# Optimization experiments

Hardware: AMD Instinct MI355X
Metric: run time of the kernel (lower is better)

The kernel has to match this reference:

```python
import jax, jax.numpy as jnp
import numpy as np

N_NODES = 50000
N_EDGES = 600000
D_IN = 128
D_HID = 128


def _sage_conv(x, src, dst, W_l, b_l, W_r):
    """PyG SAGEConv (mean aggr): out = lin_l(mean_{j in N(i)} x_j) + lin_r(x_i).
    bias lives in lin_l only."""
    n = x.shape[0]
    agg = jax.ops.segment_sum(x[src], dst, num_segments=n)            # [N, D]
    cnt = jax.ops.segment_sum(jnp.ones((src.shape[0],), x.dtype), dst, num_segments=n)
    mean = agg / jnp.maximum(cnt, 1.0)[:, None]
    return mean @ W_l.T + b_l + x @ W_r.T


def setup_inputs() -> dict:
    key = jax.random.key(0)
    ks = jax.random.split(key, 8)
    glorot = lambda k, o, i: jax.random.normal(k, (o, i), jnp.float32) * np.sqrt(2.0 / (o + i))
    return {
        "x": jax.random.normal(ks[0], (N_NODES, D_IN), jnp.float32),
        "edge_index": jax.random.randint(ks[1], (2, N_EDGES), 0, N_NODES, jnp.int64),
        "W1_l": glorot(ks[2], D_HID, D_IN),
        "b1": jnp.zeros((D_HID,), jnp.float32),
        "W1_r": glorot(ks[3], D_HID, D_IN),
        "W2_l": glorot(ks[4], D_HID, D_HID),
        "b2": jnp.zeros((D_HID,), jnp.float32),
        "W2_r": glorot(ks[5], D_HID, D_HID),
    }


def reference(x, edge_index, W1_l, b1, W1_r, W2_l, b2, W2_r):
    src, dst = edge_index[0], edge_index[1]
    h = _sage_conv(x, src, dst, W1_l, b1, W1_r)
    h = jax.nn.leaky_relu(h, negative_slope=0.2)
    return _sage_conv(h, src, dst, W2_l, b2, W2_r)
```

## Files before the change

kernel.cpp:

```cpp
#include <hip/hip_runtime.h>

#define N_NODES 50000
#define N_EDGES 600000
#define D 128
#define CAP 32
#define NTILES (N_NODES / 16)

typedef __attribute__((ext_vector_type(8))) short bf16x8;
typedef __attribute__((ext_vector_type(4))) float floatx4;
typedef __attribute__((ext_vector_type(2))) float f32x2;

__device__ inline unsigned int f2bf(float f) {
    unsigned int u = __float_as_uint(f);
    return (u + 0x7FFFu + ((u >> 16) & 1u)) >> 16;
}
__device__ inline float bf_lo(unsigned int u) { return __uint_as_float(u << 16); }
__device__ inline float bf_hi(unsigned int u) { return __uint_as_float(u & 0xFFFF0000u); }

__global__ void k_prep(const float* __restrict__ x, unsigned short* __restrict__ xbf,
                       const float* __restrict__ wa, const float* __restrict__ wb,
                       const float* __restrict__ wc, const float* __restrict__ wd,
                       unsigned short* __restrict__ wbf,
                       const int* __restrict__ src, const int* __restrict__ dst,
                       int* __restrict__ cnt, unsigned short* __restrict__ buf,
                       int* __restrict__ spillN, unsigned int* __restrict__ spillP) {
    const int b = blockIdx.x;
    const int t = threadIdx.x;
    if (b < 586) {
        int idx = b * 256 + t;
        if (idx * 4 < N_EDGES) {
            int4 dv = ((const int4*)dst)[idx];
            int4 sv = ((const int4*)src)[idx];
            int p0 = atomicAdd(&cnt[dv.x], 1);
            int p1 = atomicAdd(&cnt[dv.y], 1);
            int p2 = atomicAdd(&cnt[dv.z], 1);
            int p3 = atomicAdd(&cnt[dv.w], 1);
            if (p0 < CAP) buf[(size_t)dv.x * CAP + p0] = (unsigned short)sv.x;
            else { int k = atomicAdd(spillN, 1); spillP[k] = ((unsigned)dv.x << 16) | (unsigned)sv.x; }
            if (p1 < CAP) buf[(size_t)dv.y * CAP + p1] = (unsigned short)sv.y;
            else { int k = atomicAdd(spillN, 1); spillP[k] = ((unsigned)dv.y << 16) | (unsigned)sv.y; }
            if (p2 < CAP) buf[(size_t)dv.z * CAP + p2] = (unsigned short)sv.z;
            else { int k = atomicAdd(spillN, 1); spillP[k] = ((unsigned)dv.z << 16) | (unsigned)sv.z; }
            if (p3 < CAP) buf[(size_t)dv.w * CAP + p3] = (unsigned short)sv.w;
            else { int k = atomicAdd(spillN, 1); spillP[k] = ((unsigned)dv.w << 16) | (unsigned)sv.w; }
        }
    } else if (b < 6836) {
        int i = (b - 586) * 256 + t;
        float4 v = ((const float4*)x)[i];
        uint2 o;
        o.x = f2bf(v.x) | (f2bf(v.y) << 16);
        o.y = f2bf(v.z) | (f2bf(v.w) << 16);
        ((uint2*)xbf)[i] = o;
    } else {
        int i = (b - 6836) * 256 + t;
        const float* srcs[4] = {wa, wb, wc, wd};
        wbf[i] = (unsigned short)f2bf(srcs[i >> 14][i & 16383]);
    }
}

#define ACC8(vv) do { \
    acc[0] += bf_lo((vv).x); acc[1] += bf_hi((vv).x); \
    acc[2] += bf_lo((vv).y); acc[3] += bf_hi((vv).y); \
    acc[4] += bf_lo((vv).z); acc[5] += bf_hi((vv).z); \
    acc[6] += bf_lo((vv).w); acc[7] += bf_hi((vv).w); } while (0)

#define ACCF8(vv) do { \
    f32x2 p0 = __builtin_amdgcn_cvt_pk_f32_fp8((vv).x, false); \
    f32x2 p1 = __builtin_amdgcn_cvt_pk_f32_fp8((vv).x, true);  \
    f32x2 p2 = __builtin_amdgcn_cvt_pk_f32_fp8((vv).y, false); \
    f32x2 p3 = __builtin_amdgcn_cvt_pk_f32_fp8((vv).y, true);  \
    acc[0] += p0.x; acc[1] += p0.y; acc[2] += p1.x; acc[3] += p1.y; \
    acc[4] += p2.x; acc[5] += p2.y; acc[6] += p3.x; acc[7] += p3.y; } while (0)

template <bool RELU, bool OUT_BF16, bool WRITE_FP8, bool GATHER_FP8>
__global__ void __launch_bounds__(256) k_gather_layer(
    const int* __restrict__ cnt, const unsigned short* __restrict__ buf,
    const int* __restrict__ spillN, const unsigned int* __restrict__ spillP,
    const unsigned char* __restrict__ X8,
    const unsigned short* __restrict__ Xbf,
    const unsigned short* __restrict__ Wlbf, const float* __restrict__ bias,
    const unsigned short* __restrict__ Wrbf, void* __restrict__ outp,
    unsigned char* __restrict__ out8) {
    __shared__ unsigned short tile[16][136];

    const int t = threadIdx.x;
    const int node0 = blockIdx.x * 16;

    {
        const int nl = t >> 4, q = t & 15;
        const int node = node0 + nl;
        const int deg = cnt[node];
        const int m = deg < CAP ? deg : CAP;
        const unsigned short* __restrict__ nb = buf + (size_t)node * CAP;
        float acc[8] = {0.f, 0.f, 0.f, 0.f, 0.f, 0.f, 0.f, 0.f};
        int e = 0;
        if (GATHER_FP8) {
            for (; e + 8 <= m; e += 8) {
                uint2 v[8];
#pragma unroll
                for (int u = 0; u < 8; ++u)
                    v[u] = *(const uint2*)(X8 + (size_t)nb[e + u] * D + q * 8);
#pragma unroll
                for (int u = 0; u < 8; ++u) ACCF8(v[u]);
            }
            for (; e + 4 <= m; e += 4) {
                uint2 v[4];
#pragma unroll
                for (int u = 0; u < 4; ++u)
                    v[u] = *(const uint2*)(X8 + (size_t)nb[e + u] * D + q * 8);
#pragma unroll
                for (int u = 0; u < 4; ++u) ACCF8(v[u]);
            }
            for (; e < m; ++e) {
                uint2 v = *(const uint2*)(X8 + (size_t)nb[e] * D + q * 8);
                ACCF8(v);
            }
        } else {
            for (; e + 8 <= m; e += 8) {
                uint4 v[8];
#pragma unroll
                for (int u = 0; u < 8; ++u)
                    v[u] = *(const uint4*)(Xbf + (size_t)nb[e + u] * D + q * 8);
#pragma unroll
                for (int u = 0; u < 8; ++u) ACC8(v[u]);
            }
            for (; e + 4 <= m; e += 4) {
                uint4 v[4];
#pragma unroll
                for (int u = 0; u < 4; ++u)
                    v[u] = *(const uint4*)(Xbf + (size_t)nb[e + u] * D + q * 8);
#pragma unroll
                for (int u = 0; u < 4; ++u) ACC8(v[u]);
            }
            for (; e < m; ++e) {
                uint4 v = *(const uint4*)(Xbf + (size_t)nb[e] * D + q * 8);
                ACC8(v);
            }
        }
        if (deg > CAP) {
            int sn = *spillN;
            for (int k = 0; k < sn; ++k) {
                unsigned int p = spillP[k];
                if ((int)(p >> 16) == node) {
                    uint4 v = *(const uint4*)(Xbf + (size_t)(p & 0xFFFFu) * D + q * 8);
                    ACC8(v);
                }
            }
        }
        float inv = (deg > 0) ? 1.0f / (float)deg : 0.0f;
        uint4 o;
        o.x = f2bf(acc[0] * inv) | (f2bf(acc[1] * inv) << 16);
        o.y = f2bf(acc[2] * inv) | (f2bf(acc[3] * inv) << 16);
        o.z = f2bf(acc[4] * inv) | (f2bf(acc[5] * inv) << 16);
        o.w = f2bf(acc[6] * inv) | (f2bf(acc[7] * inv) << 16);
        *(uint4*)(&tile[nl][q * 8]) = o;
    }
    __syncthreads();

    const int lane = t & 63;
    const int wv = t >> 6;
    const int l15 = lane & 15;
    const int quad = lane >> 4;

    floatx4 c0 = (floatx4)(0.f), c1 = (floatx4)(0.f);
    const int nf0 = wv * 2, nf1 = wv * 2 + 1;

    const unsigned short* mrow = &tile[l15][quad * 8];
    const unsigned short* arowX = Xbf + (size_t)(node0 + l15) * D + quad * 8;

#pragma unroll
    for (int kk = 0; kk < 4; ++kk) {
        bf16x8 a = *(const bf16x8*)(mrow + kk * 32);
        bf16x8 b0 = *(const bf16x8*)(Wlbf + (size_t)(nf0 * 16 + l15) * D + kk * 32 + quad * 8);
        bf16x8 b1 = *(const bf16x8*)(Wlbf + (size_t)(nf1 * 16 + l15) * D + kk * 32 + quad * 8);
        c0 = __builtin_amdgcn_mfma_f32_16x16x32_bf16(a, b0, c0, 0, 0, 0);
        c1 = __builtin_amdgcn_mfma_f32_16x16x32_bf16(a, b1, c1, 0, 0, 0);
    }
#pragma unroll
    for (int kk = 0; kk < 4; ++kk) {
        bf16x8 a = *(const bf16x8*)(arowX + kk * 32);
        bf16x8 b0 = *(const bf16x8*)(Wrbf + (size_t)(nf0 * 16 + l15) * D + kk * 32 + quad * 8);
        bf16x8 b1 = *(const bf16x8*)(Wrbf + (size_t)(nf1 * 16 + l15) * D + kk * 32 + quad * 8);
        c0 = __builtin_amdgcn_mfma_f32_16x16x32_bf16(a, b0, c0, 0, 0, 0);
        c1 = __builtin_amdgcn_mfma_f32_16x16x32_bf16(a, b1, c1, 0, 0, 0);
    }

#pragma unroll
    for (int j = 0; j < 2; ++j) {
        floatx4 c = j ? c1 : c0;
        int f = (wv * 2 + j) * 16 + l15;
        float bv = bias[f];
#pragma unroll
        for (int r = 0; r < 4; ++r) {
            float v = c[r] + bv;
            if (RELU) v = v > 0.f ? v : 0.2f * v;
            int node = node0 + quad * 4 + r;
            if (OUT_BF16)
                ((unsigned short*)outp)[(size_t)node * D + f] = (unsigned short)f2bf(v);
            else
                ((float*)outp)[(size_t)node * D + f] = v;
            if (WRITE_FP8) {
                int pk = __builtin_amdgcn_cvt_pk_fp8_f32(v, v, 0, false);
                out8[(size_t)node * D + f] = (unsigned char)(pk & 0xFF);
            }
        }
    }
}


extern "C" void kernel_launch(void* const* d_in, const int* in_sizes, int n_in,
                              void* d_out, int out_size, void* d_ws, size_t ws_size,
                              hipStream_t stream) {
    (void)in_sizes; (void)n_in; (void)out_size; (void)ws_size;

    const float* x   = (const float*)d_in[0];
    const int*   ei  = (const int*)d_in[1];
    const float* W1l = (const float*)d_in[2];
    const float* b1  = (const float*)d_in[3];
    const float* W1r = (const float*)d_in[4];
    const float* W2l = (const float*)d_in[5];
    const float* b2  = (const float*)d_in[6];
    const float* W2r = (const float*)d_in[7];

    const int* src = ei;
    const int* dst = ei + N_EDGES;

    char* ws = (char*)d_ws;
    int* cnt              = (int*)(ws + 0);
    int* spillN           = (int*)(ws + 200000);
    unsigned int* spillP  = (unsigned int*)(ws + 200064);
    unsigned short* buf   = (unsigned short*)(ws + 2600064);
    unsigned short* wbf   = (unsigned short*)(ws + 5800064);
    unsigned short* hbf   = (unsigned short*)(ws + 5931136);
    unsigned char* h8     = (unsigned char*)(ws + 18731136);

    unsigned short* xbf = (unsigned short*)d_out;
    float* out = (float*)d_out;

    unsigned short* w1l_bf = wbf;
    unsigned short* w1r_bf = wbf + 16384;
    unsigned short* w2l_bf = wbf + 32768;
    unsigned short* w2r_bf = wbf + 49152;

    hipMemsetAsync(ws, 0, 200064, stream);

    k_prep<<<7092, 256, 0, stream>>>(x, xbf, W1l, W1r, W2l, W2r, wbf,
                                     src, dst, cnt, buf, spillN, spillP);

    k_gather_layer<true, true, true, false><<<NTILES, 256, 0, stream>>>(
        cnt, buf, spillN, spillP, nullptr, xbf, w1l_bf, b1, w1r_bf, (void*)hbf, h8);
    k_gather_layer<false, false, false, true><<<NTILES, 256, 0, stream>>>(
        cnt, buf, spillN, spillP, h8, hbf, w2l_bf, b2, w2r_bf, (void*)out, nullptr);
}
```

Measured before the change: 217.7 us.

## Gather FP8 in both layers and read root features from fp32 in place

Layer 1 now gathers neighbour features from an FP8 copy of x instead of bf16, halving gather bytes. The root term reads x or h directly as fp32 and converts to bf16 in registers. The layer-1 output h is written as fp32 into the output buffer, and layer 2 then overwrites that buffer in place; a __syncthreads after the MFMA loads keeps this safe within a block. This drops the bf16 x copy and the bf16 h buffer, at the cost of lower precision in the first-layer aggregation and larger fp32 root reads.

```diff
diff --git a/kernel.cpp b/kernel.cpp
--- a/kernel.cpp
+++ b/kernel.cpp
@@ -14,10 +14,19 @@
     unsigned int u = __float_as_uint(f);
     return (u + 0x7FFFu + ((u >> 16) & 1u)) >> 16;
 }
-__device__ inline float bf_lo(unsigned int u) { return __uint_as_float(u << 16); }
-__device__ inline float bf_hi(unsigned int u) { return __uint_as_float(u & 0xFFFF0000u); }
-
-__global__ void k_prep(const float* __restrict__ x, unsigned short* __restrict__ xbf,
+
+__device__ inline bf16x8 frag_from_f32(const float* p) {
+    float4 a = *(const float4*)(p);
+    float4 b = *(const float4*)(p + 4);
+    bf16x8 r;
+    r[0] = (short)f2bf(a.x); r[1] = (short)f2bf(a.y);
+    r[2] = (short)f2bf(a.z); r[3] = (short)f2bf(a.w);
+    r[4] = (short)f2bf(b.x); r[5] = (short)f2bf(b.y);
+    r[6] = (short)f2bf(b.z); r[7] = (short)f2bf(b.w);
+    return r;
+}
+
+__global__ void k_prep(const float* __restrict__ x, unsigned char* __restrict__ x8,
                        const float* __restrict__ wa, const float* __restrict__ wb,
                        const float* __restrict__ wc, const float* __restrict__ wd,
                        unsigned short* __restrict__ wbf,
@@ -47,22 +56,15 @@
     } else if (b < 6836) {
         int i = (b - 586) * 256 + t;
         float4 v = ((const float4*)x)[i];
-        uint2 o;
-        o.x = f2bf(v.x) | (f2bf(v.y) << 16);
-        o.y = f2bf(v.z) | (f2bf(v.w) << 16);
-        ((uint2*)xbf)[i] = o;
+        int lo = __builtin_amdgcn_cvt_pk_fp8_f32(v.x, v.y, 0, false);
+        int pk = __builtin_amdgcn_cvt_pk_fp8_f32(v.z, v.w, lo, true);
+        ((unsigned int*)x8)[i] = (unsigned int)pk;
     } else {
         int i = (b - 6836) * 256 + t;
         const float* srcs[4] = {wa, wb, wc, wd};
         wbf[i] = (unsigned short)f2bf(srcs[i >> 14][i & 16383]);
     }
 }
-
-#define ACC8(vv) do { \
-    acc[0] += bf_lo((vv).x); acc[1] += bf_hi((vv).x); \
-    acc[2] += bf_lo((vv).y); acc[3] += bf_hi((vv).y); \
-    acc[4] += bf_lo((vv).z); acc[5] += bf_hi((vv).z); \
-    acc[6] += bf_lo((vv).w); acc[7] += bf_hi((vv).w); } while (0)
 
 #define ACCF8(vv) do { \
     f32x2 p0 = __builtin_amdgcn_cvt_pk_f32_fp8((vv).x, false); \
@@ -72,14 +74,15 @@
     acc[0] += p0.x; acc[1] += p0.y; acc[2] += p1.x; acc[3] += p1.y; \
     acc[4] += p2.x; acc[5] += p2.y; acc[6] += p3.x; acc[7] += p3.y; } while (0)
 
-template <bool RELU, bool OUT_BF16, bool WRITE_FP8, bool GATHER_FP8>
+template <bool RELU, bool WRITE_FP8>
 __global__ void __launch_bounds__(256) k_gather_layer(
     const int* __restrict__ cnt, const unsigned short* __restrict__ buf,
     const int* __restrict__ spillN, const unsigned int* __restrict__ spillP,
     const unsigned char* __restrict__ X8,
-    const unsigned short* __restrict__ Xbf,
+    const float* Xf,
     const unsigned short* __restrict__ Wlbf, const float* __restrict__ bias,
-    const unsigned short* __restrict__ Wrbf, void* __restrict__ outp,
+    const unsigned short* __restrict__ Wrbf,
+    float* outF,
     unsigned char* __restrict__ out8) {
     __shared__ unsigned short tile[16][136];
 
@@ -94,56 +97,33 @@
         const unsigned short* __restrict__ nb = buf + (size_t)node * CAP;
         float acc[8] = {0.f, 0.f, 0.f, 0.f, 0.f, 0.f, 0.f, 0.f};
         int e = 0;
-        if (GATHER_FP8) {
-            for (; e + 8 <= m; e += 8) {
-                uint2 v[8];
-#pragma unroll
-                for (int u = 0; u < 8; ++u)
-                    v[u] = *(const uint2*)(X8 + (size_t)nb[e + u] * D + q * 8);
-#pragma unroll
-                for (int u = 0; u < 8; ++u) ACCF8(v[u]);
-            }
-            for (; e + 4 <= m; e += 4) {
-                uint2 v[4];
-#pragma unroll
-                for (int u = 0; u < 4; ++u)
-                    v[u] = *(const uint2*)(X8 + (size_t)nb[e + u] * D + q * 8);
-#pragma unroll
-                for (int u = 0; u < 4; ++u) ACCF8(v[u]);
-            }
-            for (; e < m; ++e) {
-                uint2 v = *(const uint2*)(X8 + (size_t)nb[e] * D + q * 8);
-                ACCF8(v);
-            }
-        } else {
-            for (; e + 8 <= m; e += 8) {
-                uint4 v[8];
-#pragma unroll
-                for (int u = 0; u < 8; ++u)
-                    v[u] = *(const uint4*)(Xbf + (size_t)nb[e + u] * D + q * 8);
-#pragma unroll
-                for (int u = 0; u < 8; ++u) ACC8(v[u]);
-            }
-            for (; e + 4 <= m; e += 4) {
-                uint4 v[4];
-#pragma unroll
-                for (int u = 0; u < 4; ++u)
-                    v[u] = *(const uint4*)(Xbf + (size_t)nb[e + u] * D + q * 8);
-#pragma unroll
-                for (int u = 0; u < 4; ++u) ACC8(v[u]);
-            }
-            for (; e < m; ++e) {
-                uint4 v = *(const uint4*)(Xbf + (size_t)nb[e] * D + q * 8);
-                ACC8(v);
-            }
+        for (; e + 8 <= m; e += 8) {
+            uint2 v[8];
+#pragma unroll
+            for (int u = 0; u < 8; ++u)
+                v[u] = *(const uint2*)(X8 + (size_t)nb[e + u] * D + q * 8);
+#pragma unroll
+            for (int u = 0; u < 8; ++u) ACCF8(v[u]);
+        }
+        for (; e + 4 <= m; e += 4) {
+            uint2 v[4];
+#pragma unroll
+            for (int u = 0; u < 4; ++u)
+                v[u] = *(const uint2*)(X8 + (size_t)nb[e + u] * D + q * 8);
+#pragma unroll
+            for (int u = 0; u < 4; ++u) ACCF8(v[u]);
+        }
+        for (; e < m; ++e) {
+            uint2 v = *(const uint2*)(X8 + (size_t)nb[e] * D + q * 8);
+            ACCF8(v);
         }
         if (deg > CAP) {
             int sn = *spillN;
             for (int k = 0; k < sn; ++k) {
                 unsigned int p = spillP[k];
                 if ((int)(p >> 16) == node) {
-                    uint4 v = *(const uint4*)(Xbf + (size_t)(p & 0xFFFFu) * D + q * 8);
-                    ACC8(v);
+                    uint2 v = *(const uint2*)(X8 + (size_t)(p & 0xFFFFu) * D + q * 8);
+                    ACCF8(v);
                 }
             }
         }
@@ -166,7 +146,11 @@
     const int nf0 = wv * 2, nf1 = wv * 2 + 1;
 
     const unsigned short* mrow = &tile[l15][quad * 8];
-    const unsigned short* arowX = Xbf + (size_t)(node0 + l15) * D + quad * 8;
+    const float* arow = Xf + (size_t)(node0 + l15) * D + quad * 8;
+
+    bf16x8 aX[4];
+#pragma unroll
+    for (int kk = 0; kk < 4; ++kk) aX[kk] = frag_from_f32(arow + kk * 32);
 
 #pragma unroll
     for (int kk = 0; kk < 4; ++kk) {
@@ -178,12 +162,13 @@
     }
 #pragma unroll
     for (int kk = 0; kk < 4; ++kk) {
-        bf16x8 a = *(const bf16x8*)(arowX + kk * 32);
         bf16x8 b0 = *(const bf16x8*)(Wrbf + (size_t)(nf0 * 16 + l15) * D + kk * 32 + quad * 8);
         bf16x8 b1 = *(const bf16x8*)(Wrbf + (size_t)(nf1 * 16 + l15) * D + kk * 32 + quad * 8);
-        c0 = __builtin_amdgcn_mfma_f32_16x16x32_bf16(a, b0, c0, 0, 0, 0);
-        c1 = __builtin_amdgcn_mfma_f32_16x16x32_bf16(a, b1, c1, 0, 0, 0);
-    }
+        c0 = __builtin_amdgcn_mfma_f32_16x16x32_bf16(aX[kk], b0, c0, 0, 0, 0);
+        c1 = __builtin_amdgcn_mfma_f32_16x16x32_bf16(aX[kk], b1, c1, 0, 0, 0);
+    }
+
+    __syncthreads();
 
 #pragma unroll
     for (int j = 0; j < 2; ++j) {
@@ -195,10 +180,7 @@
             float v = c[r] + bv;
             if (RELU) v = v > 0.f ? v : 0.2f * v;
             int node = node0 + quad * 4 + r;
-            if (OUT_BF16)
-                ((unsigned short*)outp)[(size_t)node * D + f] = (unsigned short)f2bf(v);
-            else
-                ((float*)outp)[(size_t)node * D + f] = v;
+            outF[(size_t)node * D + f] = v;
             if (WRITE_FP8) {
                 int pk = __builtin_amdgcn_cvt_pk_fp8_f32(v, v, 0, false);
                 out8[(size_t)node * D + f] = (unsigned char)(pk & 0xFF);
@@ -231,10 +213,10 @@
     unsigned int* spillP  = (unsigned int*)(ws + 200064);
     unsigned short* buf   = (unsigned short*)(ws + 2600064);
     unsigned short* wbf   = (unsigned short*)(ws + 5800064);
-    unsigned short* hbf   = (unsigned short*)(ws + 5931136);
-    unsigned char* h8     = (unsigned char*)(ws + 18731136);
-
-    unsigned short* xbf = (unsigned short*)d_out;
+    unsigned char* x8     = (unsigned char*)(ws + 5931136);
+    unsigned char* h8     = (unsigned char*)(ws + 12331136);
+
+    float* hf  = (float*)d_out;
     float* out = (float*)d_out;
 
     unsigned short* w1l_bf = wbf;
@@ -244,11 +226,11 @@
 
     hipMemsetAsync(ws, 0, 200064, stream);
 
-    k_prep<<<7092, 256, 0, stream>>>(x, xbf, W1l, W1r, W2l, W2r, wbf,
+    k_prep<<<7092, 256, 0, stream>>>(x, x8, W1l, W1r, W2l, W2r, wbf,
                                      src, dst, cnt, buf, spillN, spillP);
 
-    k_gather_layer<true, true, true, false><<<NTILES, 256, 0, stream>>>(
-        cnt, buf, spillN, spillP, nullptr, xbf, w1l_bf, b1, w1r_bf, (void*)hbf, h8);
-    k_gather_layer<false, false, false, true><<<NTILES, 256, 0, stream>>>(
-        cnt, buf, spillN, spillP, h8, hbf, w2l_bf, b2, w2r_bf, (void*)out, nullptr);
-}
+    k_gather_layer<true, true><<<NTILES, 256, 0, stream>>>(
+        cnt, buf, spillN, spillP, x8, x, w1l_bf, b1, w1r_bf, hf, h8);
+    k_gather_layer<false, false><<<NTILES, 256, 0, stream>>>(
+        cnt, buf, spillN, spillP, h8, hf, w2l_bf, b2, w2r_bf, out, nullptr);
+}
```

After: 224.2 us. 3.0% more time.
